# Performance work log

Hardware: AMD Instinct MI355X
Metric: run time of the kernel (lower is better)

The kernel has to match this reference:

```python
import jax, jax.numpy as jnp
import numpy as np

HIDDEN = 2048
N_HEADS = 16
N_KV = 2
HEAD_DIM = 256
ROT_DIM = 64  # partial_rotary_factor 0.25
EPS = 1e-6
B, S = 2, 2048


def _rms_norm(x, w, eps=EPS):
    var = jnp.mean(jnp.square(x), axis=-1, keepdims=True)
    return x * jax.lax.rsqrt(var + eps) * w


def _rotate_half(x):
    x1, x2 = jnp.split(x, 2, axis=-1)
    return jnp.concatenate([-x2, x1], axis=-1)


def setup_inputs() -> dict:
    key = jax.random.key(0)
    ks = jax.random.split(key, 8)
    hidden_states = jax.random.normal(ks[0], (B, S, HIDDEN), dtype=jnp.float32)
    # real RoPE cos/sin over rotary_dim (HF convention: freqs duplicated)
    inv_freq = 1.0 / (10000.0 ** (np.arange(0, ROT_DIM, 2, dtype=np.float32) / ROT_DIM))
    pos = np.arange(S, dtype=np.float32)
    ang = np.einsum('s,f->sf', pos, inv_freq)                # [S, ROT_DIM/2]
    emb = np.concatenate([ang, ang], axis=-1)                # [S, ROT_DIM]
    cos = jnp.asarray(np.broadcast_to(np.cos(emb), (B, S, ROT_DIM)))
    sin = jnp.asarray(np.broadcast_to(np.sin(emb), (B, S, ROT_DIM)))
    sc = 0.02
    Wq = jax.random.normal(ks[1], (N_HEADS * HEAD_DIM * 2, HIDDEN), dtype=jnp.float32) * sc
    Wk = jax.random.normal(ks[2], (N_KV * HEAD_DIM, HIDDEN), dtype=jnp.float32) * sc
    Wv = jax.random.normal(ks[3], (N_KV * HEAD_DIM, HIDDEN), dtype=jnp.float32) * sc
    Wo = jax.random.normal(ks[4], (HIDDEN, N_HEADS * HEAD_DIM), dtype=jnp.float32) * sc
    q_norm_w = jnp.ones((HEAD_DIM,), dtype=jnp.float32)
    k_norm_w = jnp.ones((HEAD_DIM,), dtype=jnp.float32)
    return {"hidden_states": hidden_states, "cos": cos, "sin": sin,
            "Wq": Wq, "Wk": Wk, "Wv": Wv, "Wo": Wo,
            "q_norm_w": q_norm_w, "k_norm_w": k_norm_w}


def reference(hidden_states, cos, sin, Wq, Wk, Wv, Wo, q_norm_w, k_norm_w):
    b, s, _ = hidden_states.shape
    # gated Q projection: [b, s, n_heads, 2*head_dim] -> query, gate
    qg = jnp.einsum('bsd,od->bso', hidden_states, Wq).reshape(b, s, N_HEADS, 2 * HEAD_DIM)
    q, gate = jnp.split(qg, 2, axis=-1)                      # each [b,s,H,D]
    gate = gate.reshape(b, s, N_HEADS * HEAD_DIM)
    k = jnp.einsum('bsd,od->bso', hidden_states, Wk).reshape(b, s, N_KV, HEAD_DIM)
    v = jnp.einsum('bsd,od->bso', hidden_states, Wv).reshape(b, s, N_KV, HEAD_DIM)
    # per-head RMSNorm before RoPE
    q = _rms_norm(q, q_norm_w)
    k = _rms_norm(k, k_norm_w)
    # partial RoPE on first ROT_DIM dims
    c = cos[:, :, None, :]
    sn = sin[:, :, None, :]
    q_rot, q_pass = q[..., :ROT_DIM], q[..., ROT_DIM:]
    k_rot, k_pass = k[..., :ROT_DIM], k[..., ROT_DIM:]
    q_rot = q_rot * c + _rotate_half(q_rot) * sn
    k_rot = k_rot * c + _rotate_half(k_rot) * sn
    q = jnp.concatenate([q_rot, q_pass], axis=-1)
    k = jnp.concatenate([k_rot, k_pass], axis=-1)
    # GQA: repeat kv heads
    rep = N_HEADS // N_KV
    k = jnp.repeat(k, rep, axis=2)
    v = jnp.repeat(v, rep, axis=2)
    scale = 1.0 / jnp.sqrt(jnp.float32(HEAD_DIM))
    scores = jnp.einsum('bqhd,bkhd->bhqk', q, k) * scale
    causal = jnp.tril(jnp.ones((s, s), dtype=bool))
    scores = jnp.where(causal[None, None], scores, jnp.finfo(scores.dtype).min)
    probs = jax.nn.softmax(scores, axis=-1)
    attn = jnp.einsum('bhqk,bkhd->bqhd', probs, v).reshape(b, s, N_HEADS * HEAD_DIM)
    attn = attn * jax.nn.sigmoid(gate)
    return jnp.einsum('bsi,oi->bso', attn, Wo)
```

## Files before the change

### kernel.cpp

```cpp
#include <hip/hip_runtime.h>
#include <stdint.h>

typedef unsigned short u16;
typedef __bf16 bf16x8 __attribute__((ext_vector_type(8)));
typedef float f32x4 __attribute__((ext_vector_type(4)));
typedef u16 u16x4 __attribute__((ext_vector_type(4)));
typedef u16 u16x8 __attribute__((ext_vector_type(8)));

__device__ __forceinline__ u16 f2b(float f) {
    unsigned u = __builtin_bit_cast(unsigned, f);
    u = u + 0x7FFFu + ((u >> 16) & 1u);
    return (u16)(u >> 16);
}
__device__ __forceinline__ float b2f(u16 b) {
    return __builtin_bit_cast(float, (unsigned)b << 16);
}

__device__ __forceinline__ void glds16(const u16* g, u16* l) {
    __builtin_amdgcn_global_load_lds(
        (const __attribute__((address_space(1))) void*)g,
        (__attribute__((address_space(3))) void*)l,
        16, 0, 0);
}

__global__ __launch_bounds__(256) void cast_bf16(const float* __restrict__ src,
                                                 u16* __restrict__ dst, int n) {
    int i = (blockIdx.x * 256 + threadIdx.x) * 4;
    if (i >= n) return;
    f32x4 v = *(const f32x4*)(src + i);
    u16x4 o;
    o.x = f2b(v.x); o.y = f2b(v.y); o.z = f2b(v.z); o.w = f2b(v.w);
    *(u16x4*)(dst + i) = o;
}

template <int OUT_BF16>
__global__ __launch_bounds__(256) void gemm_bt(const u16* __restrict__ A,
                                               const u16* __restrict__ Bt,
                                               void* __restrict__ Cout,
                                               int M, int N, int K) {
    __shared__ u16 As[128 * 32];
    __shared__ u16 Bs[128 * 32];
    const int tid  = threadIdx.x;
    const int w    = tid >> 6;
    const int lane = tid & 63;
    const int quad = lane >> 4;
    const int ml   = lane & 15;
    const long bm  = (long)blockIdx.y * 128;
    const long bn  = (long)blockIdx.x * 128;
    const int wm   = (w >> 1) * 64;
    const int wn   = (w & 1) * 64;
    const int grow = lane >> 2;
    const int gcol = (lane & 3) * 8;

    const u16* Ag = A  + (bm + w * 16 + grow) * (long)K + gcol;
    const u16* Bg = Bt + (bn + w * 16 + grow) * (long)K + gcol;
    u16* lAs0 = &As[(w * 16) * 32];
    u16* lAs1 = &As[(64 + w * 16) * 32];
    u16* lBs0 = &Bs[(w * 16) * 32];
    u16* lBs1 = &Bs[(64 + w * 16) * 32];

    const f32x4 fz = {0.f, 0.f, 0.f, 0.f};
    f32x4 acc[4][4];
#pragma unroll
    for (int i = 0; i < 4; ++i)
#pragma unroll
        for (int j = 0; j < 4; ++j) acc[i][j] = fz;

    for (int k0 = 0; k0 < K; k0 += 32) {
        __syncthreads();
        glds16(Ag + k0,               lAs0);
        glds16(Ag + 64 * (long)K + k0, lAs1);
        glds16(Bg + k0,               lBs0);
        glds16(Bg + 64 * (long)K + k0, lBs1);
        __builtin_amdgcn_s_waitcnt(0);
        __syncthreads();
        bf16x8 af[4], bfr[4];
#pragma unroll
        for (int mt = 0; mt < 4; ++mt)
            af[mt] = *(const bf16x8*)&As[(wm + mt * 16 + ml) * 32 + quad * 8];
#pragma unroll
        for (int nt = 0; nt < 4; ++nt)
            bfr[nt] = *(const bf16x8*)&Bs[(wn + nt * 16 + ml) * 32 + quad * 8];
#pragma unroll
        for (int mt = 0; mt < 4; ++mt)
#pragma unroll
            for (int nt = 0; nt < 4; ++nt)
                acc[mt][nt] = __builtin_amdgcn_mfma_f32_16x16x32_bf16(
                    af[mt], bfr[nt], acc[mt][nt], 0, 0, 0);
    }
#pragma unroll
    for (int mt = 0; mt < 4; ++mt)
#pragma unroll
        for (int nt = 0; nt < 4; ++nt)
#pragma unroll
            for (int r = 0; r < 4; ++r) {
                long row = bm + wm + mt * 16 + quad * 4 + r;
                long col = bn + wn + nt * 16 + ml;
                float v = acc[mt][nt][r];
                if (OUT_BF16) ((u16*)Cout)[row * N + col] = f2b(v);
                else          ((float*)Cout)[row * N + col] = v;
            }
}

__global__ __launch_bounds__(64) void norm_rope(const u16* __restrict__ qgk,
                                                const float* __restrict__ cosp,
                                                const float* __restrict__ sinp,
                                                const float* __restrict__ qw,
                                                const float* __restrict__ kw,
                                                u16* __restrict__ qf,
                                                u16* __restrict__ kf) {
    const int t = blockIdx.x;
    const int u = blockIdx.y;
    const int lane = threadIdx.x;
    const int b = t >> 11, s = t & 2047;
    const u16* src; const float* wgt; u16* dst;
    if (u < 16) {
        src = qgk + (long)t * 8704 + u * 512;
        wgt = qw;
        dst = qf + ((long)(b * 16 + u) * 2048 + s) * 256;
    } else {
        int kh = u - 16;
        src = qgk + (long)t * 8704 + 8192 + kh * 256;
        wgt = kw;
        dst = kf + ((long)(b * 2 + kh) * 2048 + s) * 256;
    }
    const int d0 = lane * 4;
    u16x4 raw = *(const u16x4*)(src + d0);
    float x0 = b2f(raw.x), x1 = b2f(raw.y), x2 = b2f(raw.z), x3 = b2f(raw.w);
    float ss = x0 * x0 + x1 * x1 + x2 * x2 + x3 * x3;
    for (int off = 32; off; off >>= 1) ss += __shfl_xor(ss, off, 64);
    float inv = rsqrtf(ss * (1.0f / 256.0f) + 1e-6f);
    float n0 = x0 * inv * wgt[d0 + 0];
    float n1 = x1 * inv * wgt[d0 + 1];
    float n2 = x2 * inv * wgt[d0 + 2];
    float n3 = x3 * inv * wgt[d0 + 3];
    float p0 = __shfl_xor(n0, 8, 64);
    float p1 = __shfl_xor(n1, 8, 64);
    float p2 = __shfl_xor(n2, 8, 64);
    float p3 = __shfl_xor(n3, 8, 64);
    if (lane < 16) {
        f32x4 c  = *(const f32x4*)(cosp + (long)t * 64 + d0);
        f32x4 sn = *(const f32x4*)(sinp + (long)t * 64 + d0);
        float sgn = (lane < 8) ? -1.f : 1.f;
        n0 = n0 * c[0] + sgn * p0 * sn[0];
        n1 = n1 * c[1] + sgn * p1 * sn[1];
        n2 = n2 * c[2] + sgn * p2 * sn[2];
        n3 = n3 * c[3] + sgn * p3 * sn[3];
    }
    const float qs = (u < 16) ? 0.0625f : 1.0f;
    n0 *= qs; n1 *= qs; n2 *= qs; n3 *= qs;
    u16x4 o;
    o.x = f2b(n0); o.y = f2b(n1); o.z = f2b(n2); o.w = f2b(n3);
    *(u16x4*)(dst + d0) = o;
}

__global__ __launch_bounds__(256, 2) void attn_fused(const u16* __restrict__ qf,
                                                     const u16* __restrict__ kf,
                                                     const u16* __restrict__ vt,
                                                     const u16* __restrict__ qgk,
                                                     u16* __restrict__ attn_g) {
    __shared__ u16 Ks[64 * 264];
    __shared__ u16 Vt[256 * 72];
    __shared__ u16 P[64 * 72];
    const int flat = blockIdx.x;
    const int qt = 31 - (flat >> 5);
    const int h  = flat & 15;
    const int b  = (flat >> 4) & 1;
    const int kh = h >> 3;
    const int tid = threadIdx.x;
    const int w = tid >> 6, lane = tid & 63;
    const int quad = lane >> 4, ml = lane & 15;
    const int qbase = qt * 64;
    const int qrow = qbase + w * 16;

    const u16* qptr = qf + ((long)(b * 16 + h) * 2048 + qrow + ml) * 256;
    bf16x8 qfrag[8];
#pragma unroll
    for (int dd = 0; dd < 8; ++dd)
        qfrag[dd] = *(const bf16x8*)(qptr + dd * 32 + quad * 8);

    const f32x4 fz = {0.f, 0.f, 0.f, 0.f};
    f32x4 oacc[16];
#pragma unroll
    for (int i = 0; i < 16; ++i) oacc[i] = fz;
    float lsum[4] = {0.f, 0.f, 0.f, 0.f};

    const u16* kbp = kf + (long)(b * 2 + kh) * 2048 * 256;
    const long vbase = (long)kh * 256 * 4096 + (long)b * 2048;

    u16x8 Kreg[8], Vreg[8];
#pragma unroll
    for (int i = 0; i < 8; ++i) {
        int c = i * 256 + tid;
        Kreg[i] = *(const u16x8*)(kbp + (long)(c >> 5) * 256 + (c & 31) * 8);
        Vreg[i] = *(const u16x8*)(vt + vbase + (long)(c >> 3) * 4096 + (c & 7) * 8);
    }

    const int nkt = qt + 1;
    for (int kt = 0; kt < nkt; ++kt) {
        __syncthreads();
#pragma unroll
        for (int i = 0; i < 8; ++i) {
            int c = i * 256 + tid;
            *(u16x8*)&Ks[(c >> 5) * 264 + (c & 31) * 8] = Kreg[i];
            *(u16x8*)&Vt[(c >> 3) * 72 + (c & 7) * 8]   = Vreg[i];
        }
        __syncthreads();
        if (kt + 1 < nkt) {
            const int kb2 = (kt + 1) * 64;
#pragma unroll
            for (int i = 0; i < 8; ++i) {
                int c = i * 256 + tid;
                Kreg[i] = *(const u16x8*)(kbp + (long)(kb2 + (c >> 5)) * 256 + (c & 31) * 8);
                Vreg[i] = *(const u16x8*)(vt + vbase + (long)(c >> 3) * 4096 + kb2 + (c & 7) * 8);
            }
        }

        f32x4 sacc[4];
#pragma unroll
        for (int i = 0; i < 4; ++i) sacc[i] = fz;
#pragma unroll
        for (int dd = 0; dd < 8; ++dd) {
            bf16x8 kf0 = *(const bf16x8*)&Ks[(0 * 16 + ml) * 264 + dd * 32 + quad * 8];
            bf16x8 kf1 = *(const bf16x8*)&Ks[(1 * 16 + ml) * 264 + dd * 32 + quad * 8];
            bf16x8 kf2 = *(const bf16x8*)&Ks[(2 * 16 + ml) * 264 + dd * 32 + quad * 8];
            bf16x8 kf3 = *(const bf16x8*)&Ks[(3 * 16 + ml) * 264 + dd * 32 + quad * 8];
            sacc[0] = __builtin_amdgcn_mfma_f32_16x16x32_bf16(qfrag[dd], kf0, sacc[0], 0, 0, 0);
            sacc[1] = __builtin_amdgcn_mfma_f32_16x16x32_bf16(qfrag[dd], kf1, sacc[1], 0, 0, 0);
            sacc[2] = __builtin_amdgcn_mfma_f32_16x16x32_bf16(qfrag[dd], kf2, sacc[2], 0, 0, 0);
            sacc[3] = __builtin_amdgcn_mfma_f32_16x16x32_bf16(qfrag[dd], kf3, sacc[3], 0, 0, 0);
        }

        const bool diag = (kt == qt);
#pragma unroll
        for (int nt = 0; nt < 4; ++nt)
#pragma unroll
            for (int r = 0; r < 4; ++r) {
                float sv = sacc[nt][r];
                if (diag) {
                    int col = nt * 16 + ml;
                    int row = w * 16 + quad * 4 + r;
                    sv = (col > row) ? -1e30f : sv;
                }
                float pv = __expf(sv - 16.0f);
                lsum[r] += pv;
                P[(w * 16 + quad * 4 + r) * 72 + nt * 16 + ml] = f2b(pv);
            }

#pragma unroll
        for (int ks = 0; ks < 2; ++ks) {
            bf16x8 pfrag = *(const bf16x8*)&P[(w * 16 + ml) * 72 + ks * 32 + quad * 8];
#pragma unroll
            for (int dt = 0; dt < 16; ++dt) {
                bf16x8 vfrag = *(const bf16x8*)&Vt[(dt * 16 + ml) * 72 + ks * 32 + quad * 8];
                oacc[dt] = __builtin_amdgcn_mfma_f32_16x16x32_bf16(pfrag, vfrag, oacc[dt], 0, 0, 0);
            }
        }
    }

#pragma unroll
    for (int off = 1; off < 16; off <<= 1)
#pragma unroll
        for (int r = 0; r < 4; ++r) lsum[r] += __shfl_xor(lsum[r], off, 64);

#pragma unroll
    for (int dt = 0; dt < 16; ++dt)
#pragma unroll
        for (int r = 0; r < 4; ++r) {
            int srow = qrow + quad * 4 + r;
            long tok = (long)b * 2048 + srow;
            int d = dt * 16 + ml;
            float o = oacc[dt][r] / lsum[r];
            float g = b2f(qgk[tok * 8704 + h * 512 + 256 + d]);
            float gv = o / (1.f + __expf(-g));
            attn_g[tok * 4096 + h * 256 + d] = f2b(gv);
        }
}

extern "C" void kernel_launch(void* const* d_in, const int* in_sizes, int n_in,
                              void* d_out, int out_size, void* d_ws, size_t ws_size,
                              hipStream_t stream) {
    (void)in_sizes; (void)n_in; (void)out_size;
    const float* hidden = (const float*)d_in[0];
    const float* cosp   = (const float*)d_in[1];
    const float* sinp   = (const float*)d_in[2];
    const float* Wq     = (const float*)d_in[3];
    const float* Wk     = (const float*)d_in[4];
    const float* Wv     = (const float*)d_in[5];
    const float* Wo     = (const float*)d_in[6];
    const float* qw     = (const float*)d_in[7];
    const float* kw     = (const float*)d_in[8];
    float* out = (float*)d_out;

    char* p = (char*)d_ws;
    u16* h_bf   = (u16*)p; p += (size_t)8388608 * 2;
    u16* Wqk_bf = (u16*)p; p += (size_t)17825792 * 2;
    u16* Wv_bf  = (u16*)p; p += (size_t)1048576 * 2;
    u16* Wo_bf  = (u16*)p; p += (size_t)8388608 * 2;
    u16* qgk    = (u16*)p; p += (size_t)35651584 * 2;
    u16* v_t    = (u16*)p; p += (size_t)2097152 * 2;
    u16* q_f    = (u16*)p; p += (size_t)16777216 * 2;
    u16* k_f    = (u16*)p; p += (size_t)2097152 * 2;
    u16* attn_g = (u16*)p; p += (size_t)16777216 * 2;
    if ((size_t)(p - (char*)d_ws) > ws_size) return;

    cast_bf16<<<8192,  256, 0, stream>>>(hidden, h_bf, 8388608);
    cast_bf16<<<16384, 256, 0, stream>>>(Wq, Wqk_bf, 16777216);
    cast_bf16<<<1024,  256, 0, stream>>>(Wk, Wqk_bf + (size_t)8192 * 2048, 1048576);
    cast_bf16<<<1024,  256, 0, stream>>>(Wv, Wv_bf, 1048576);
    cast_bf16<<<8192,  256, 0, stream>>>(Wo, Wo_bf, 8388608);

    gemm_bt<1><<<dim3(68, 32), 256, 0, stream>>>(h_bf, Wqk_bf, qgk, 4096, 8704, 2048);
    gemm_bt<1><<<dim3(32, 4), 256, 0, stream>>>(Wv_bf, h_bf, v_t, 512, 4096, 2048);

    norm_rope<<<dim3(4096, 18), 64, 0, stream>>>(qgk, cosp, sinp, qw, kw, q_f, k_f);

    attn_fused<<<dim3(1024), 256, 0, stream>>>(q_f, k_f, v_t, qgk, attn_g);

    gemm_bt<0><<<dim3(16, 32), 256, 0, stream>>>(attn_g, Wo_bf, out, 4096, 2048, 4096);
}
```

Baseline: 678.7 us.

## Enlarge attention Q tile to 128 rows with direct-to-LDS swizzled K/V loads

The fused attention kernel now processes 128 query rows per block, with each wave owning two 16-row M tiles, so every K/V tile staged in LDS is reused twice as much and the grid halves to 512 blocks. K and V are loaded with global_load_lds into XOR-swizzled unpadded LDS buffers instead of being prefetched through registers, and the P buffer aliases the K buffer to save LDS. Division is replaced with hardware reciprocals. In exchange, the register-prefetch overlap is lost (each tile's load is waited on with waitcnt(0)), an extra barrier is added, and there are fewer blocks for load balancing across the causal triangle.

```diff
diff --git a/kernel.cpp b/kernel.cpp
--- a/kernel.cpp
+++ b/kernel.cpp
@@ -159,122 +159,145 @@
                                                      const u16* __restrict__ vt,
                                                      const u16* __restrict__ qgk,
                                                      u16* __restrict__ attn_g) {
-    __shared__ u16 Ks[64 * 264];
-    __shared__ u16 Vt[256 * 72];
-    __shared__ u16 P[64 * 72];
+    __shared__ u16 Ks[64 * 256];
+    __shared__ u16 Vt[256 * 64];
+    u16* Pb = Ks;
     const int flat = blockIdx.x;
-    const int qt = 31 - (flat >> 5);
+    const int qt = 15 - (flat >> 5);
     const int h  = flat & 15;
     const int b  = (flat >> 4) & 1;
     const int kh = h >> 3;
     const int tid = threadIdx.x;
     const int w = tid >> 6, lane = tid & 63;
     const int quad = lane >> 4, ml = lane & 15;
-    const int qbase = qt * 64;
-    const int qrow = qbase + w * 16;
-
-    const u16* qptr = qf + ((long)(b * 16 + h) * 2048 + qrow + ml) * 256;
-    bf16x8 qfrag[8];
-#pragma unroll
-    for (int dd = 0; dd < 8; ++dd)
-        qfrag[dd] = *(const bf16x8*)(qptr + dd * 32 + quad * 8);
+    const int qbase = qt * 128;
+
+    bf16x8 qfrag[2][8];
+#pragma unroll
+    for (int mt = 0; mt < 2; ++mt) {
+        const u16* qp = qf + ((long)(b * 16 + h) * 2048 + qbase + w * 32 + mt * 16 + ml) * 256;
+#pragma unroll
+        for (int dd = 0; dd < 8; ++dd)
+            qfrag[mt][dd] = *(const bf16x8*)(qp + dd * 32 + quad * 8);
+    }
 
     const f32x4 fz = {0.f, 0.f, 0.f, 0.f};
-    f32x4 oacc[16];
-#pragma unroll
-    for (int i = 0; i < 16; ++i) oacc[i] = fz;
-    float lsum[4] = {0.f, 0.f, 0.f, 0.f};
+    f32x4 oacc[2][16];
+#pragma unroll
+    for (int mt = 0; mt < 2; ++mt)
+#pragma unroll
+        for (int i = 0; i < 16; ++i) oacc[mt][i] = fz;
+    float lsum[2][4] = {{0.f,0.f,0.f,0.f},{0.f,0.f,0.f,0.f}};
 
     const u16* kbp = kf + (long)(b * 2 + kh) * 2048 * 256;
     const long vbase = (long)kh * 256 * 4096 + (long)b * 2048;
 
-    u16x8 Kreg[8], Vreg[8];
-#pragma unroll
-    for (int i = 0; i < 8; ++i) {
-        int c = i * 256 + tid;
-        Kreg[i] = *(const u16x8*)(kbp + (long)(c >> 5) * 256 + (c & 31) * 8);
-        Vreg[i] = *(const u16x8*)(vt + vbase + (long)(c >> 3) * 4096 + (c & 7) * 8);
-    }
-
-    const int nkt = qt + 1;
+    const int nkt = 2 * qt + 2;
     for (int kt = 0; kt < nkt; ++kt) {
+        const int kb = kt * 64;
         __syncthreads();
 #pragma unroll
         for (int i = 0; i < 8; ++i) {
-            int c = i * 256 + tid;
-            *(u16x8*)&Ks[(c >> 5) * 264 + (c & 31) * 8] = Kreg[i];
-            *(u16x8*)&Vt[(c >> 3) * 72 + (c & 7) * 8]   = Vreg[i];
+            int s = w * 8 + i;
+            {
+                int keyl = 2 * s + (lane >> 5);
+                int c = (lane & 31) ^ (keyl & 7);
+                glds16(kbp + (long)(kb + keyl) * 256 + c * 8, &Ks[s * 512]);
+            }
+            {
+                int dl = 8 * s + (lane >> 3);
+                int c = (lane & 7) ^ (dl & 7);
+                glds16(vt + vbase + (long)dl * 4096 + kb + c * 8, &Vt[s * 512]);
+            }
         }
-        __syncthreads();
-        if (kt + 1 < nkt) {
-            const int kb2 = (kt + 1) * 64;
-#pragma unroll
-            for (int i = 0; i < 8; ++i) {
-                int c = i * 256 + tid;
-                Kreg[i] = *(const u16x8*)(kbp + (long)(kb2 + (c >> 5)) * 256 + (c & 31) * 8);
-                Vreg[i] = *(const u16x8*)(vt + vbase + (long)(c >> 3) * 4096 + kb2 + (c & 7) * 8);
+        __builtin_amdgcn_s_waitcnt(0);
+        __syncthreads();
+
+        f32x4 sacc[2][4];
+#pragma unroll
+        for (int mt = 0; mt < 2; ++mt)
+#pragma unroll
+            for (int nt = 0; nt < 4; ++nt) sacc[mt][nt] = fz;
+#pragma unroll
+        for (int dd = 0; dd < 8; ++dd) {
+#pragma unroll
+            for (int nt = 0; nt < 4; ++nt) {
+                bf16x8 kfr = *(const bf16x8*)&Ks[(nt * 16 + ml) * 256 +
+                                                 (((dd * 4 + quad) ^ (ml & 7)) * 8)];
+                sacc[0][nt] = __builtin_amdgcn_mfma_f32_16x16x32_bf16(qfrag[0][dd], kfr, sacc[0][nt], 0, 0, 0);
+                sacc[1][nt] = __builtin_amdgcn_mfma_f32_16x16x32_bf16(qfrag[1][dd], kfr, sacc[1][nt], 0, 0, 0);
             }
         }
-
-        f32x4 sacc[4];
-#pragma unroll
-        for (int i = 0; i < 4; ++i) sacc[i] = fz;
-#pragma unroll
-        for (int dd = 0; dd < 8; ++dd) {
-            bf16x8 kf0 = *(const bf16x8*)&Ks[(0 * 16 + ml) * 264 + dd * 32 + quad * 8];
-            bf16x8 kf1 = *(const bf16x8*)&Ks[(1 * 16 + ml) * 264 + dd * 32 + quad * 8];
-            bf16x8 kf2 = *(const bf16x8*)&Ks[(2 * 16 + ml) * 264 + dd * 32 + quad * 8];
-            bf16x8 kf3 = *(const bf16x8*)&Ks[(3 * 16 + ml) * 264 + dd * 32 + quad * 8];
-            sacc[0] = __builtin_amdgcn_mfma_f32_16x16x32_bf16(qfrag[dd], kf0, sacc[0], 0, 0, 0);
-            sacc[1] = __builtin_amdgcn_mfma_f32_16x16x32_bf16(qfrag[dd], kf1, sacc[1], 0, 0, 0);
-            sacc[2] = __builtin_amdgcn_mfma_f32_16x16x32_bf16(qfrag[dd], kf2, sacc[2], 0, 0, 0);
-            sacc[3] = __builtin_amdgcn_mfma_f32_16x16x32_bf16(qfrag[dd], kf3, sacc[3], 0, 0, 0);
+        __syncthreads();
+
+#pragma unroll
+        for (int mt = 0; mt < 2; ++mt) {
+            const int base_mt = qbase + w * 32 + mt * 16;
+            const int prow = (w * 32 + mt * 16 + quad * 4) * 88;
+            if (kb + 63 > base_mt) {
+#pragma unroll
+                for (int nt = 0; nt < 4; ++nt)
+#pragma unroll
+                    for (int r = 0; r < 4; ++r) {
+                        int col = kb + nt * 16 + ml;
+                        int row = base_mt + quad * 4 + r;
+                        float sv = (col > row) ? -1e30f : sacc[mt][nt][r];
+                        float pv = __expf(sv - 16.0f);
+                        lsum[mt][r] += pv;
+                        Pb[prow + r * 88 + nt * 16 + ml] = f2b(pv);
+                    }
+            } else {
+#pragma unroll
+                for (int nt = 0; nt < 4; ++nt)
+#pragma unroll
+                    for (int r = 0; r < 4; ++r) {
+                        float pv = __expf(sacc[mt][nt][r] - 16.0f);
+                        lsum[mt][r] += pv;
+                        Pb[prow + r * 88 + nt * 16 + ml] = f2b(pv);
+                    }
+            }
         }
 
-        const bool diag = (kt == qt);
-#pragma unroll
-        for (int nt = 0; nt < 4; ++nt)
+#pragma unroll
+        for (int ks = 0; ks < 2; ++ks) {
+            bf16x8 pf0 = *(const bf16x8*)&Pb[(w * 32 + ml) * 88 + ks * 32 + quad * 8];
+            bf16x8 pf1 = *(const bf16x8*)&Pb[(w * 32 + 16 + ml) * 88 + ks * 32 + quad * 8];
+#pragma unroll
+            for (int dt = 0; dt < 16; ++dt) {
+                bf16x8 vfr = *(const bf16x8*)&Vt[(dt * 16 + ml) * 64 +
+                                                 (((ks * 4 + quad) ^ (ml & 7)) * 8)];
+                oacc[0][dt] = __builtin_amdgcn_mfma_f32_16x16x32_bf16(pf0, vfr, oacc[0][dt], 0, 0, 0);
+                oacc[1][dt] = __builtin_amdgcn_mfma_f32_16x16x32_bf16(pf1, vfr, oacc[1][dt], 0, 0, 0);
+            }
+        }
+    }
+
+#pragma unroll
+    for (int off = 1; off < 16; off <<= 1)
+#pragma unroll
+        for (int mt = 0; mt < 2; ++mt)
+#pragma unroll
+            for (int r = 0; r < 4; ++r) lsum[mt][r] += __shfl_xor(lsum[mt][r], off, 64);
+    float invl[2][4];
+#pragma unroll
+    for (int mt = 0; mt < 2; ++mt)
+#pragma unroll
+        for (int r = 0; r < 4; ++r) invl[mt][r] = __builtin_amdgcn_rcpf(lsum[mt][r]);
+
+#pragma unroll
+    for (int mt = 0; mt < 2; ++mt)
+#pragma unroll
+        for (int dt = 0; dt < 16; ++dt)
 #pragma unroll
             for (int r = 0; r < 4; ++r) {
-                float sv = sacc[nt][r];
-                if (diag) {
-                    int col = nt * 16 + ml;
-                    int row = w * 16 + quad * 4 + r;
-                    sv = (col > row) ? -1e30f : sv;
-                }
-                float pv = __expf(sv - 16.0f);
-                lsum[r] += pv;
-                P[(w * 16 + quad * 4 + r) * 72 + nt * 16 + ml] = f2b(pv);
-            }
-
-#pragma unroll
-        for (int ks = 0; ks < 2; ++ks) {
-            bf16x8 pfrag = *(const bf16x8*)&P[(w * 16 + ml) * 72 + ks * 32 + quad * 8];
-#pragma unroll
-            for (int dt = 0; dt < 16; ++dt) {
-                bf16x8 vfrag = *(const bf16x8*)&Vt[(dt * 16 + ml) * 72 + ks * 32 + quad * 8];
-                oacc[dt] = __builtin_amdgcn_mfma_f32_16x16x32_bf16(pfrag, vfrag, oacc[dt], 0, 0, 0);
-            }
-        }
-    }
-
-#pragma unroll
-    for (int off = 1; off < 16; off <<= 1)
-#pragma unroll
-        for (int r = 0; r < 4; ++r) lsum[r] += __shfl_xor(lsum[r], off, 64);
-
-#pragma unroll
-    for (int dt = 0; dt < 16; ++dt)
-#pragma unroll
-        for (int r = 0; r < 4; ++r) {
-            int srow = qrow + quad * 4 + r;
-            long tok = (long)b * 2048 + srow;
-            int d = dt * 16 + ml;
-            float o = oacc[dt][r] / lsum[r];
-            float g = b2f(qgk[tok * 8704 + h * 512 + 256 + d]);
-            float gv = o / (1.f + __expf(-g));
-            attn_g[tok * 4096 + h * 256 + d] = f2b(gv);
-        }
+                int srow = qbase + w * 32 + mt * 16 + quad * 4 + r;
+                long tok = (long)b * 2048 + srow;
+                int d = dt * 16 + ml;
+                float o = oacc[mt][dt][r] * invl[mt][r];
+                float g = b2f(qgk[tok * 8704 + h * 512 + 256 + d]);
+                float gv = o * __builtin_amdgcn_rcpf(1.f + __expf(-g));
+                attn_g[tok * 4096 + h * 256 + d] = f2b(gv);
+            }
 }
 
 extern "C" void kernel_launch(void* const* d_in, const int* in_sizes, int n_in,
@@ -315,7 +338,7 @@
 
     norm_rope<<<dim3(4096, 18), 64, 0, stream>>>(qgk, cosp, sinp, qw, kw, q_f, k_f);
 
-    attn_fused<<<dim3(1024), 256, 0, stream>>>(q_f, k_f, v_t, qgk, attn_g);
+    attn_fused<<<dim3(512), 256, 0, stream>>>(q_f, k_f, v_t, qgk, attn_g);
 
     gemm_bt<0><<<dim3(16, 32), 256, 0, stream>>>(attn_g, Wo_bf, out, 4096, 2048, 4096);
 }
```

Result: slower. 787.0 us (+15.9%).
